# Kernel tuning notes

Hardware: AMD Instinct MI355X
Metric: run time of the kernel (lower is better)

## Reference

```python
import jax, jax.numpy as jnp
import numpy as np

B, L, E, H = 1, 2048, 512, 8
D = E // H


def setup_inputs() -> dict:
    key = jax.random.key(0)
    k0, k1, k2 = jax.random.split(key, 3)
    x = jax.random.normal(k0, (B, L, E), jnp.float32)
    W_qkv = jax.random.normal(k1, (E, 3 * E), jnp.float32) / np.sqrt(E).astype(np.float32)
    b_qkv = jnp.zeros((3 * E,), jnp.float32)
    W_out = jax.random.normal(k2, (E, E), jnp.float32) / np.sqrt(E).astype(np.float32)
    b_out = jnp.zeros((E,), jnp.float32)
    return {"x": x, "W_qkv": W_qkv, "b_qkv": b_qkv, "W_out": W_out, "b_out": b_out}


def reference(x, W_qkv, b_qkv, W_out, b_out):
    num_heads = H
    eps = 1e-6
    b, l, e = x.shape
    d = e // num_heads
    qkv = x @ W_qkv + b_qkv                      # [B, L, 3E]
    q, k, v = jnp.split(qkv, 3, axis=-1)
    q = q.reshape(b, l, num_heads, d).transpose(0, 2, 1, 3)  # [B,H,L,D]
    k = k.reshape(b, l, num_heads, d).transpose(0, 2, 1, 3)
    v = v.reshape(b, l, num_heads, d).transpose(0, 2, 1, 3)
    pos = jnp.arange(l, dtype=jnp.float32).reshape(1, 1, l, 1)
    cos_w = jnp.cos(jnp.pi / 2 * pos / l)
    sin_w = jnp.sin(jnp.pi / 2 * pos / l)
    q_prime = jax.nn.relu(q)
    k_prime = jax.nn.relu(k)

    def branch(w):
        qw = q_prime * w                          # [B,H,L,D]
        kw = k_prime * w
        kv = jnp.einsum('bhld,bhle->bhlde', kw, v)  # causal running KV state
        kv_cum = jnp.cumsum(kv, axis=2)
        ctx = jnp.einsum('bhld,bhlde->bhle', qw, kv_cum)
        nrm = jnp.einsum('bhld,bhld->bhl', qw, jnp.cumsum(kw, axis=2))
        return ctx, nrm

    ctx_cos, nrm_cos = branch(cos_w)
    ctx_sin, nrm_sin = branch(sin_w)
    out = (ctx_cos + ctx_sin) / ((nrm_cos + nrm_sin)[..., None] + eps)
    out = out.transpose(0, 2, 1, 3).reshape(b, l, e)
    return out @ W_out + b_out
```

## Files before the change

### kernel.cpp

```cpp
#include <hip/hip_runtime.h>

constexpr int L_SEQ = 2048;
constexpr int E_DIM = 512;
constexpr int H_NUM = 8;
constexpr int QKV_W = 3 * E_DIM;
constexpr int NC = 32;
constexpr float PI_HALF = 1.5707963267948966f;

typedef __attribute__((ext_vector_type(8))) short bf16x8;
typedef __attribute__((ext_vector_type(4))) float f32x4;
typedef __attribute__((ext_vector_type(4))) short short4v;

__device__ __forceinline__ short f2bf(float f) {
  union { float f; unsigned int u; } v; v.f = f;
  unsigned int r = v.u + 0x7fffu + ((v.u >> 16) & 1u);
  return (short)(r >> 16);
}
__device__ __forceinline__ float bf2f(short s) {
  union { unsigned int u; float f; } v;
  v.u = ((unsigned int)(unsigned short)s) << 16;
  return v.f;
}

__device__ __forceinline__ void glds16(const void* g, void* l) {
  __builtin_amdgcn_global_load_lds(
      (const __attribute__((address_space(1))) unsigned int*)g,
      (__attribute__((address_space(3))) unsigned int*)l, 16, 0, 0);
}

template <int WTM, int WTN, bool OB>
__global__ __launch_bounds__(256) void gemm_mfma_bf16(
    const short* __restrict__ A, const short* __restrict__ Bt,
    const float* __restrict__ bias, void* __restrict__ Cout,
    int M, int N, int K) {
  constexpr int BM = WTM * 32;
  constexpr int BN = WTN * 32;
  __shared__ short As[BM * 32];
  __shared__ short Bs[BN * 32];

  const int t = threadIdx.x;
  const int wave = t >> 6;
  const int lane = t & 63;
  const int quad = lane >> 4;
  const int lr = lane & 15;

  const int row0 = blockIdx.y * BM;
  const int col0 = blockIdx.x * BN;
  const int wrow = (wave >> 1) * (BM / 2);
  const int wcol = (wave & 1) * (BN / 2);

  f32x4 acc[WTM][WTN];
#pragma unroll
  for (int m = 0; m < WTM; ++m)
#pragma unroll
    for (int n = 0; n < WTN; ++n) acc[m][n] = (f32x4){0.f, 0.f, 0.f, 0.f};

  for (int k0 = 0; k0 < K; k0 += 32) {
#pragma unroll
    for (int p = wave; p < BM / 16; p += 4) {
      const int idx = p * 64 + lane;
      glds16(A + (size_t)(row0 + (idx >> 2)) * K + k0 + (idx & 3) * 8, As + p * 512);
    }
#pragma unroll
    for (int p = wave; p < BN / 16; p += 4) {
      const int idx = p * 64 + lane;
      glds16(Bt + (size_t)(col0 + (idx >> 2)) * K + k0 + (idx & 3) * 8, Bs + p * 512);
    }
    __syncthreads();

    bf16x8 af[WTM], bf_[WTN];
#pragma unroll
    for (int m = 0; m < WTM; ++m)
      af[m] = *(const bf16x8*)(As + (wrow + m * 16 + lr) * 32 + quad * 8);
#pragma unroll
    for (int n = 0; n < WTN; ++n)
      bf_[n] = *(const bf16x8*)(Bs + (wcol + n * 16 + lr) * 32 + quad * 8);
#pragma unroll
    for (int m = 0; m < WTM; ++m)
#pragma unroll
      for (int n = 0; n < WTN; ++n)
        acc[m][n] = __builtin_amdgcn_mfma_f32_16x16x32_bf16(af[m], bf_[n], acc[m][n], 0, 0, 0);
    __syncthreads();
  }

#pragma unroll
  for (int m = 0; m < WTM; ++m) {
#pragma unroll
    for (int n = 0; n < WTN; ++n) {
      const int col = col0 + wcol + n * 16 + lr;
      const int rowb = row0 + wrow + m * 16 + quad * 4;
      const float bb = bias[col];
#pragma unroll
      for (int r = 0; r < 4; ++r) {
        const float val = acc[m][n][r] + bb;
        if (OB)
          ((short*)Cout)[(size_t)(rowb + r) * N + col] = f2bf(val);
        else
          ((float*)Cout)[(size_t)(rowb + r) * N + col] = val;
      }
    }
  }
}

__global__ __launch_bounds__(256) void prep_kernel(
    const float* __restrict__ x, const float* __restrict__ W_qkv,
    const float* __restrict__ W_out, short* __restrict__ xb,
    short* __restrict__ Wqkv_t, short* __restrict__ Wout_t) {
  const int b = blockIdx.x;
  if (b < 1024) {
    const int i = b * 256 + threadIdx.x;
    const float4 v = ((const float4*)x)[i];
    short4v o;
    o.x = f2bf(v.x); o.y = f2bf(v.y); o.z = f2bf(v.z); o.w = f2bf(v.w);
    ((short4v*)xb)[i] = o;
    return;
  }
  __shared__ float tile[32][33];
  const float* W; short* Wt; int R, Cc, c0, r0;
  if (b < 1792) {
    const int bb = b - 1024;
    W = W_qkv; Wt = Wqkv_t; R = E_DIM; Cc = QKV_W;
    c0 = (bb % 48) * 32; r0 = (bb / 48) * 32;
  } else {
    const int bb = b - 1792;
    W = W_out; Wt = Wout_t; R = E_DIM; Cc = E_DIM;
    c0 = (bb % 16) * 32; r0 = (bb / 16) * 32;
  }
  const int tx = threadIdx.x & 31, ty = threadIdx.x >> 5;
  for (int i = ty; i < 32; i += 8) tile[i][tx] = W[(size_t)(r0 + i) * Cc + c0 + tx];
  __syncthreads();
  for (int i = ty; i < 32; i += 8)
    Wt[(size_t)(c0 + i) * R + r0 + tx] = f2bf(tile[tx][i]);
}

__global__ __launch_bounds__(256) void chunk_kv_mfma(
    const short* __restrict__ qkvb, short* __restrict__ Sb, float* __restrict__ ksum) {
  const int c = blockIdx.x, h = blockIdx.y;
  __shared__ short kT[128][72];
  __shared__ short vT[64][72];
  const int t = threadIdx.x;
  const int w = t >> 6, lane = t & 63, lr = lane & 15, quad = lane >> 4;

#pragma unroll
  for (int r = 0; r < 16; ++r) {
    const int i = w + 4 * r, d = lane;
    const short* row = qkvb + (size_t)(c * 64 + i) * QKV_W;
    const float kv_ = fmaxf(bf2f(row[E_DIM + h * 64 + d]), 0.f);
    const float v_ = bf2f(row[2 * E_DIM + h * 64 + d]);
    const float th = PI_HALF * (float)(c * 64 + i) / (float)L_SEQ;
    kT[d][i] = f2bf(kv_ * __cosf(th));
    kT[64 + d][i] = f2bf(kv_ * __sinf(th));
    vT[d][i] = f2bf(v_);
  }
  __syncthreads();

  f32x4 acc[8];
#pragma unroll
  for (int n = 0; n < 8; ++n) acc[n] = (f32x4){0.f, 0.f, 0.f, 0.f};
#pragma unroll
  for (int kk = 0; kk < 2; ++kk) {
    const bf16x8 av = *(const bf16x8*)&vT[16 * w + lr][kk * 32 + quad * 8];
#pragma unroll
    for (int n = 0; n < 8; ++n) {
      const bf16x8 bv = *(const bf16x8*)&kT[16 * n + lr][kk * 32 + quad * 8];
      acc[n] = __builtin_amdgcn_mfma_f32_16x16x32_bf16(av, bv, acc[n], 0, 0, 0);
    }
  }

  short* Sc = Sb + ((size_t)(h * NC + c)) * 8192;
#pragma unroll
  for (int n = 0; n < 8; ++n) {
    const int dd = 16 * n + lr;
#pragma unroll
    for (int r = 0; r < 4; ++r) {
      const int e = 16 * w + quad * 4 + r;
      Sc[(size_t)e * 128 + dd] = f2bf(acc[n][r]);
    }
  }

  if (t < 128) {
    float s = 0.f;
#pragma unroll
    for (int j = 0; j < 8; ++j) {
      const bf16x8 kv8 = *(const bf16x8*)&kT[t][j * 8];
#pragma unroll
      for (int q = 0; q < 8; ++q) s += bf2f(kv8[q]);
    }
    ksum[(size_t)(h * NC + c) * 128 + t] = s;
  }
}

__global__ __launch_bounds__(256) void scan_kernel(
    const short* __restrict__ Sb, short* __restrict__ Spb,
    const float* __restrict__ ksum, float* __restrict__ ksumP) {
  const int h = blockIdx.y;
  const int g = (blockIdx.x * 256 + threadIdx.x) * 8;
  float run[8];
#pragma unroll
  for (int q = 0; q < 8; ++q) run[q] = 0.f;
#pragma unroll
  for (int c = 0; c < NC; ++c) {
    const size_t off = ((size_t)(h * NC + c)) * 8192 + g;
    const bf16x8 v8 = *(const bf16x8*)(Sb + off);
    bf16x8 o;
#pragma unroll
    for (int q = 0; q < 8; ++q) o[q] = f2bf(run[q]);
    *(bf16x8*)(Spb + off) = o;
#pragma unroll
    for (int q = 0; q < 8; ++q) run[q] += bf2f(v8[q]);
  }
  if (blockIdx.x == 0 && threadIdx.x < 128) {
    const int d = threadIdx.x;
    float r2 = 0.f;
#pragma unroll
    for (int c = 0; c < NC; ++c) {
      const size_t off = (size_t)(h * NC + c) * 128 + d;
      ksumP[off] = r2;
      r2 += ksum[off];
    }
  }
}

__global__ __launch_bounds__(256) void chunk_out_mfma(
    const short* __restrict__ qkvb, const short* __restrict__ Spb,
    const float* __restrict__ ksumP, short* __restrict__ attn) {
  const int c = blockIdx.x, h = blockIdx.y;
  __shared__ short Qc[64][136];
  __shared__ short Kc[64][136];
  __shared__ short Am[64][72];
  __shared__ short vT[64][72];
  __shared__ float nrmP[64][4];
  __shared__ float nrmA[64];
  const int t = threadIdx.x;
  const int w = t >> 6, lane = t & 63, lr = lane & 15, quad = lane >> 4;

#pragma unroll
  for (int r = 0; r < 16; ++r) {
    const int i = w + 4 * r, d = lane;
    const short* row = qkvb + (size_t)(c * 64 + i) * QKV_W;
    const float q_ = fmaxf(bf2f(row[h * 64 + d]), 0.f);
    const float k_ = fmaxf(bf2f(row[E_DIM + h * 64 + d]), 0.f);
    const float v_ = bf2f(row[2 * E_DIM + h * 64 + d]);
    const float th = PI_HALF * (float)(c * 64 + i) / (float)L_SEQ;
    const float cw = __cosf(th), sw = __sinf(th);
    Qc[i][d] = f2bf(q_ * cw);
    Qc[i][64 + d] = f2bf(q_ * sw);
    Kc[i][d] = f2bf(k_ * cw);
    Kc[i][64 + d] = f2bf(k_ * sw);
    vT[d][i] = f2bf(v_);
  }
  __syncthreads();

  bf16x8 av[4];
#pragma unroll
  for (int kk = 0; kk < 4; ++kk)
    av[kk] = *(const bf16x8*)&Qc[16 * w + lr][kk * 32 + quad * 8];

  const short* Spc = Spb + ((size_t)(h * NC + c)) * 8192;
  f32x4 acc_c[4];
#pragma unroll
  for (int n = 0; n < 4; ++n) acc_c[n] = (f32x4){0.f, 0.f, 0.f, 0.f};
#pragma unroll
  for (int kk = 0; kk < 4; ++kk) {
#pragma unroll
    for (int n = 0; n < 4; ++n) {
      const bf16x8 bv = *(const bf16x8*)(Spc + (size_t)(16 * n + lr) * 128 + kk * 32 + quad * 8);
      acc_c[n] = __builtin_amdgcn_mfma_f32_16x16x32_bf16(av[kk], bv, acc_c[n], 0, 0, 0);
    }
  }

  f32x4 acc_a[4];
#pragma unroll
  for (int n = 0; n < 4; ++n) acc_a[n] = (f32x4){0.f, 0.f, 0.f, 0.f};
#pragma unroll
  for (int kk = 0; kk < 4; ++kk) {
#pragma unroll
    for (int n = 0; n < 4; ++n) {
      const bf16x8 bv = *(const bf16x8*)&Kc[16 * n + lr][kk * 32 + quad * 8];
      acc_a[n] = __builtin_amdgcn_mfma_f32_16x16x32_bf16(av[kk], bv, acc_a[n], 0, 0, 0);
    }
  }
#pragma unroll
  for (int n = 0; n < 4; ++n) {
#pragma unroll
    for (int r = 0; r < 4; ++r) {
      const int gi = 16 * w + quad * 4 + r;
      const int gj = 16 * n + lr;
      float val = (gj <= gi) ? acc_a[n][r] : 0.f;
      Am[gi][gj] = f2bf(val);
      float s = val;
      s += __shfl_xor(s, 1, 64);
      s += __shfl_xor(s, 2, 64);
      s += __shfl_xor(s, 4, 64);
      s += __shfl_xor(s, 8, 64);
      if (lr == 0) nrmP[gi][n] = s;
    }
  }
  __syncthreads();

#pragma unroll
  for (int kk = 0; kk < 2; ++kk) {
    const bf16x8 am = *(const bf16x8*)&Am[16 * w + lr][kk * 32 + quad * 8];
#pragma unroll
    for (int n = 0; n < 4; ++n) {
      const bf16x8 bv = *(const bf16x8*)&vT[16 * n + lr][kk * 32 + quad * 8];
      acc_c[n] = __builtin_amdgcn_mfma_f32_16x16x32_bf16(am, bv, acc_c[n], 0, 0, 0);
    }
  }

  {
    const int i = t >> 2, p = t & 3;
    const float* Kp = ksumP + (size_t)(h * NC + c) * 128;
    float dot = 0.f;
#pragma unroll
    for (int jj = 0; jj < 32; ++jj) {
      const int dd = p * 32 + jj;
      dot += bf2f(Qc[i][dd]) * Kp[dd];
    }
    nrmP[i][p] += dot;
  }
  __syncthreads();
  if (t < 64) nrmA[t] = nrmP[t][0] + nrmP[t][1] + nrmP[t][2] + nrmP[t][3];
  __syncthreads();

#pragma unroll
  for (int n = 0; n < 4; ++n) {
#pragma unroll
    for (int r = 0; r < 4; ++r) {
      const int gi = 16 * w + quad * 4 + r;
      const int e = 16 * n + lr;
      const float val = acc_c[n][r] / (nrmA[gi] + 1e-6f);
      attn[(size_t)(c * 64 + gi) * E_DIM + h * 64 + e] = f2bf(val);
    }
  }
}

extern "C" void kernel_launch(void* const* d_in, const int* in_sizes, int n_in,
                              void* d_out, int out_size, void* d_ws, size_t ws_size,
                              hipStream_t stream) {
  (void)in_sizes; (void)n_in; (void)out_size; (void)ws_size;
  const float* x     = (const float*)d_in[0];
  const float* W_qkv = (const float*)d_in[1];
  const float* b_qkv = (const float*)d_in[2];
  const float* W_out = (const float*)d_in[3];
  const float* b_out = (const float*)d_in[4];
  float* out = (float*)d_out;

  short* sws = (short*)d_ws;
  short* qkvb   = sws;
  short* Sb     = qkvb + 3145728;
  short* Spb    = Sb + 2097152;
  short* attn_b = Spb + 2097152;
  short* xb     = attn_b + 1048576;
  short* Wqkv_t = xb + 1048576;
  short* Wout_t = Wqkv_t + 786432;
  float* ksum   = (float*)(Wout_t + 262144);
  float* ksumP  = ksum + 32768;

  prep_kernel<<<2048, 256, 0, stream>>>(x, W_qkv, W_out, xb, Wqkv_t, Wout_t);

  gemm_mfma_bf16<2, 2, true><<<dim3(QKV_W / 64, L_SEQ / 64), 256, 0, stream>>>(
      xb, Wqkv_t, b_qkv, qkvb, L_SEQ, QKV_W, E_DIM);

  chunk_kv_mfma<<<dim3(NC, H_NUM), 256, 0, stream>>>(qkvb, Sb, ksum);

  scan_kernel<<<dim3(4, H_NUM), 256, 0, stream>>>(Sb, Spb, ksum, ksumP);

  chunk_out_mfma<<<dim3(NC, H_NUM), 256, 0, stream>>>(qkvb, Spb, ksumP, attn_b);

  gemm_mfma_bf16<1, 2, false><<<dim3(E_DIM / 64, L_SEQ / 32), 256, 0, stream>>>(
      attn_b, Wout_t, b_out, out, L_SEQ, E_DIM, E_DIM);
}
```

Baseline: 109.7 us.

## Fuse all stages into one persistent kernel with software grid barriers

After: 432.0 us. 294% more time.

```diff
diff --git a/kernel.cpp b/kernel.cpp
--- a/kernel.cpp
+++ b/kernel.cpp
@@ -5,11 +5,11 @@
 constexpr int H_NUM = 8;
 constexpr int QKV_W = 3 * E_DIM;
 constexpr int NC = 32;
+constexpr int NBLK = 512;
 constexpr float PI_HALF = 1.5707963267948966f;
 
 typedef __attribute__((ext_vector_type(8))) short bf16x8;
 typedef __attribute__((ext_vector_type(4))) float f32x4;
-typedef __attribute__((ext_vector_type(4))) short short4v;
 
 __device__ __forceinline__ short f2bf(float f) {
   union { float f; unsigned int u; } v; v.f = f;
@@ -28,24 +28,31 @@
       (__attribute__((address_space(3))) unsigned int*)l, 16, 0, 0);
 }
 
+__device__ __forceinline__ void grid_sync(unsigned* bar) {
+  __syncthreads();
+  if (threadIdx.x == 0) {
+    unsigned gen = __hip_atomic_load(&bar[1], __ATOMIC_ACQUIRE, __HIP_MEMORY_SCOPE_AGENT);
+    unsigned prev = __hip_atomic_fetch_add(&bar[0], 1u, __ATOMIC_ACQ_REL, __HIP_MEMORY_SCOPE_AGENT);
+    if (prev == (unsigned)NBLK - 1u) {
+      __hip_atomic_store(&bar[0], 0u, __ATOMIC_RELAXED, __HIP_MEMORY_SCOPE_AGENT);
+      __hip_atomic_fetch_add(&bar[1], 1u, __ATOMIC_ACQ_REL, __HIP_MEMORY_SCOPE_AGENT);
+    } else {
+      while (__hip_atomic_load(&bar[1], __ATOMIC_ACQUIRE, __HIP_MEMORY_SCOPE_AGENT) == gen)
+        __builtin_amdgcn_s_sleep(2);
+    }
+  }
+  __syncthreads();
+}
+
 template <int WTM, int WTN, bool OB>
-__global__ __launch_bounds__(256) void gemm_mfma_bf16(
+__device__ __forceinline__ void gemm_tile(
     const short* __restrict__ A, const short* __restrict__ Bt,
     const float* __restrict__ bias, void* __restrict__ Cout,
-    int M, int N, int K) {
+    int N, int K, int row0, int col0, short* As, short* Bs) {
   constexpr int BM = WTM * 32;
   constexpr int BN = WTN * 32;
-  __shared__ short As[BM * 32];
-  __shared__ short Bs[BN * 32];
-
   const int t = threadIdx.x;
-  const int wave = t >> 6;
-  const int lane = t & 63;
-  const int quad = lane >> 4;
-  const int lr = lane & 15;
-
-  const int row0 = blockIdx.y * BM;
-  const int col0 = blockIdx.x * BN;
+  const int wave = t >> 6, lane = t & 63, quad = lane >> 4, lr = lane & 15;
   const int wrow = (wave >> 1) * (BM / 2);
   const int wcol = (wave & 1) * (BN / 2);
 
@@ -102,236 +109,261 @@
   }
 }
 
-__global__ __launch_bounds__(256) void prep_kernel(
+__global__ __launch_bounds__(256, 2) void mega_kernel(
     const float* __restrict__ x, const float* __restrict__ W_qkv,
-    const float* __restrict__ W_out, short* __restrict__ xb,
-    short* __restrict__ Wqkv_t, short* __restrict__ Wout_t) {
-  const int b = blockIdx.x;
-  if (b < 1024) {
-    const int i = b * 256 + threadIdx.x;
-    const float4 v = ((const float4*)x)[i];
-    short4v o;
-    o.x = f2bf(v.x); o.y = f2bf(v.y); o.z = f2bf(v.z); o.w = f2bf(v.w);
-    ((short4v*)xb)[i] = o;
-    return;
-  }
-  __shared__ float tile[32][33];
-  const float* W; short* Wt; int R, Cc, c0, r0;
-  if (b < 1792) {
-    const int bb = b - 1024;
-    W = W_qkv; Wt = Wqkv_t; R = E_DIM; Cc = QKV_W;
-    c0 = (bb % 48) * 32; r0 = (bb / 48) * 32;
-  } else {
-    const int bb = b - 1792;
-    W = W_out; Wt = Wout_t; R = E_DIM; Cc = E_DIM;
-    c0 = (bb % 16) * 32; r0 = (bb / 16) * 32;
-  }
-  const int tx = threadIdx.x & 31, ty = threadIdx.x >> 5;
-  for (int i = ty; i < 32; i += 8) tile[i][tx] = W[(size_t)(r0 + i) * Cc + c0 + tx];
-  __syncthreads();
-  for (int i = ty; i < 32; i += 8)
-    Wt[(size_t)(c0 + i) * R + r0 + tx] = f2bf(tile[tx][i]);
-}
-
-__global__ __launch_bounds__(256) void chunk_kv_mfma(
-    const short* __restrict__ qkvb, short* __restrict__ Sb, float* __restrict__ ksum) {
-  const int c = blockIdx.x, h = blockIdx.y;
-  __shared__ short kT[128][72];
-  __shared__ short vT[64][72];
+    const float* __restrict__ b_qkv, const float* __restrict__ W_out,
+    const float* __restrict__ b_out, float* __restrict__ out,
+    short* __restrict__ xb, short* __restrict__ Wqkv_t, short* __restrict__ Wout_t,
+    short* __restrict__ qkvb, short* __restrict__ Sb, short* __restrict__ Spb,
+    short* __restrict__ attn_b, float* __restrict__ ksum, float* __restrict__ ksumP,
+    unsigned* bar) {
+  __shared__ __align__(16) char smem[49920];
+  const int bid = blockIdx.x;
   const int t = threadIdx.x;
   const int w = t >> 6, lane = t & 63, lr = lane & 15, quad = lane >> 4;
 
-#pragma unroll
-  for (int r = 0; r < 16; ++r) {
-    const int i = w + 4 * r, d = lane;
-    const short* row = qkvb + (size_t)(c * 64 + i) * QKV_W;
-    const float kv_ = fmaxf(bf2f(row[E_DIM + h * 64 + d]), 0.f);
-    const float v_ = bf2f(row[2 * E_DIM + h * 64 + d]);
-    const float th = PI_HALF * (float)(c * 64 + i) / (float)L_SEQ;
-    kT[d][i] = f2bf(kv_ * __cosf(th));
-    kT[64 + d][i] = f2bf(kv_ * __sinf(th));
-    vT[d][i] = f2bf(v_);
-  }
-  __syncthreads();
-
-  f32x4 acc[8];
-#pragma unroll
-  for (int n = 0; n < 8; ++n) acc[n] = (f32x4){0.f, 0.f, 0.f, 0.f};
-#pragma unroll
-  for (int kk = 0; kk < 2; ++kk) {
-    const bf16x8 av = *(const bf16x8*)&vT[16 * w + lr][kk * 32 + quad * 8];
-#pragma unroll
-    for (int n = 0; n < 8; ++n) {
-      const bf16x8 bv = *(const bf16x8*)&kT[16 * n + lr][kk * 32 + quad * 8];
-      acc[n] = __builtin_amdgcn_mfma_f32_16x16x32_bf16(av, bv, acc[n], 0, 0, 0);
-    }
-  }
-
-  short* Sc = Sb + ((size_t)(h * NC + c)) * 8192;
-#pragma unroll
-  for (int n = 0; n < 8; ++n) {
-    const int dd = 16 * n + lr;
-#pragma unroll
-    for (int r = 0; r < 4; ++r) {
-      const int e = 16 * w + quad * 4 + r;
-      Sc[(size_t)e * 128 + dd] = f2bf(acc[n][r]);
-    }
-  }
-
-  if (t < 128) {
-    float s = 0.f;
-#pragma unroll
-    for (int j = 0; j < 8; ++j) {
-      const bf16x8 kv8 = *(const bf16x8*)&kT[t][j * 8];
-#pragma unroll
-      for (int q = 0; q < 8; ++q) s += bf2f(kv8[q]);
-    }
-    ksum[(size_t)(h * NC + c) * 128 + t] = s;
-  }
-}
-
-__global__ __launch_bounds__(256) void scan_kernel(
-    const short* __restrict__ Sb, short* __restrict__ Spb,
-    const float* __restrict__ ksum, float* __restrict__ ksumP) {
-  const int h = blockIdx.y;
-  const int g = (blockIdx.x * 256 + threadIdx.x) * 8;
-  float run[8];
-#pragma unroll
-  for (int q = 0; q < 8; ++q) run[q] = 0.f;
-#pragma unroll
-  for (int c = 0; c < NC; ++c) {
-    const size_t off = ((size_t)(h * NC + c)) * 8192 + g;
-    const bf16x8 v8 = *(const bf16x8*)(Sb + off);
+  {
+    const int g = bid * 256 + t;
+    const float4 v0 = ((const float4*)x)[g * 2];
+    const float4 v1 = ((const float4*)x)[g * 2 + 1];
     bf16x8 o;
-#pragma unroll
-    for (int q = 0; q < 8; ++q) o[q] = f2bf(run[q]);
-    *(bf16x8*)(Spb + off) = o;
-#pragma unroll
-    for (int q = 0; q < 8; ++q) run[q] += bf2f(v8[q]);
-  }
-  if (blockIdx.x == 0 && threadIdx.x < 128) {
-    const int d = threadIdx.x;
-    float r2 = 0.f;
-#pragma unroll
-    for (int c = 0; c < NC; ++c) {
-      const size_t off = (size_t)(h * NC + c) * 128 + d;
-      ksumP[off] = r2;
-      r2 += ksum[off];
-    }
-  }
-}
-
-__global__ __launch_bounds__(256) void chunk_out_mfma(
-    const short* __restrict__ qkvb, const short* __restrict__ Spb,
-    const float* __restrict__ ksumP, short* __restrict__ attn) {
-  const int c = blockIdx.x, h = blockIdx.y;
-  __shared__ short Qc[64][136];
-  __shared__ short Kc[64][136];
-  __shared__ short Am[64][72];
-  __shared__ short vT[64][72];
-  __shared__ float nrmP[64][4];
-  __shared__ float nrmA[64];
-  const int t = threadIdx.x;
-  const int w = t >> 6, lane = t & 63, lr = lane & 15, quad = lane >> 4;
-
-#pragma unroll
-  for (int r = 0; r < 16; ++r) {
-    const int i = w + 4 * r, d = lane;
-    const short* row = qkvb + (size_t)(c * 64 + i) * QKV_W;
-    const float q_ = fmaxf(bf2f(row[h * 64 + d]), 0.f);
-    const float k_ = fmaxf(bf2f(row[E_DIM + h * 64 + d]), 0.f);
-    const float v_ = bf2f(row[2 * E_DIM + h * 64 + d]);
-    const float th = PI_HALF * (float)(c * 64 + i) / (float)L_SEQ;
-    const float cw = __cosf(th), sw = __sinf(th);
-    Qc[i][d] = f2bf(q_ * cw);
-    Qc[i][64 + d] = f2bf(q_ * sw);
-    Kc[i][d] = f2bf(k_ * cw);
-    Kc[i][64 + d] = f2bf(k_ * sw);
-    vT[d][i] = f2bf(v_);
-  }
-  __syncthreads();
-
-  bf16x8 av[4];
-#pragma unroll
-  for (int kk = 0; kk < 4; ++kk)
-    av[kk] = *(const bf16x8*)&Qc[16 * w + lr][kk * 32 + quad * 8];
-
-  const short* Spc = Spb + ((size_t)(h * NC + c)) * 8192;
-  f32x4 acc_c[4];
-#pragma unroll
-  for (int n = 0; n < 4; ++n) acc_c[n] = (f32x4){0.f, 0.f, 0.f, 0.f};
-#pragma unroll
-  for (int kk = 0; kk < 4; ++kk) {
+    o[0] = f2bf(v0.x); o[1] = f2bf(v0.y); o[2] = f2bf(v0.z); o[3] = f2bf(v0.w);
+    o[4] = f2bf(v1.x); o[5] = f2bf(v1.y); o[6] = f2bf(v1.z); o[7] = f2bf(v1.w);
+    *(bf16x8*)(xb + (size_t)g * 8) = o;
+
+    float (*tile)[33] = (float(*)[33])smem;
+    const int tx = t & 31, ty = t >> 5;
+#pragma unroll
+    for (int rep = 0; rep < 2; ++rep) {
+      const int j = bid * 2 + rep;
+      const float* W; short* Wt; int Cc, c0, r0;
+      if (j < 768) {
+        W = W_qkv; Wt = Wqkv_t; Cc = QKV_W;
+        c0 = (j % 48) * 32; r0 = (j / 48) * 32;
+      } else {
+        const int jj = j - 768;
+        W = W_out; Wt = Wout_t; Cc = E_DIM;
+        c0 = (jj % 16) * 32; r0 = (jj / 16) * 32;
+      }
+      __syncthreads();
+      for (int i = ty; i < 32; i += 8) tile[i][tx] = W[(size_t)(r0 + i) * Cc + c0 + tx];
+      __syncthreads();
+      for (int i = ty; i < 32; i += 8)
+        Wt[(size_t)(c0 + i) * E_DIM + r0 + tx] = f2bf(tile[tx][i]);
+    }
+  }
+  grid_sync(bar);
+
+  {
+    short* As = (short*)smem;
+    short* Bs = (short*)(smem + 4096);
+    const int col0 = (bid & 15) * 96;
+    const int row0 = (bid >> 4) * 64;
+    gemm_tile<2, 3, true>(xb, Wqkv_t, b_qkv, qkvb, QKV_W, E_DIM, row0, col0, As, Bs);
+  }
+  grid_sync(bar);
+
+  {
+    const int half = bid >> 8, rem = bid & 255, h = rem >> 5, c = rem & 31;
+    short (*kT)[72] = (short(*)[72])smem;
+    short (*vT)[72] = (short(*)[72])(smem + 9216);
+#pragma unroll
+    for (int r = 0; r < 16; ++r) {
+      const int i = w + 4 * r, d = lane;
+      const short* row = qkvb + (size_t)(c * 64 + i) * QKV_W;
+      const float kv_ = fmaxf(bf2f(row[E_DIM + h * 64 + d]), 0.f);
+      const float v_ = bf2f(row[2 * E_DIM + h * 64 + d]);
+      const float th = PI_HALF * (float)(c * 64 + i) / (float)L_SEQ;
+      const float wgt = half ? __sinf(th) : __cosf(th);
+      kT[d][i] = f2bf(kv_ * wgt);
+      vT[d][i] = f2bf(v_);
+    }
+    __syncthreads();
+
+    f32x4 acc[4];
+#pragma unroll
+    for (int n = 0; n < 4; ++n) acc[n] = (f32x4){0.f, 0.f, 0.f, 0.f};
+#pragma unroll
+    for (int kk = 0; kk < 2; ++kk) {
+      const bf16x8 av = *(const bf16x8*)&vT[16 * w + lr][kk * 32 + quad * 8];
+#pragma unroll
+      for (int n = 0; n < 4; ++n) {
+        const bf16x8 bv = *(const bf16x8*)&kT[16 * n + lr][kk * 32 + quad * 8];
+        acc[n] = __builtin_amdgcn_mfma_f32_16x16x32_bf16(av, bv, acc[n], 0, 0, 0);
+      }
+    }
+    short* Sc = Sb + ((size_t)(h * NC + c)) * 8192;
 #pragma unroll
     for (int n = 0; n < 4; ++n) {
-      const bf16x8 bv = *(const bf16x8*)(Spc + (size_t)(16 * n + lr) * 128 + kk * 32 + quad * 8);
-      acc_c[n] = __builtin_amdgcn_mfma_f32_16x16x32_bf16(av[kk], bv, acc_c[n], 0, 0, 0);
-    }
-  }
-
-  f32x4 acc_a[4];
-#pragma unroll
-  for (int n = 0; n < 4; ++n) acc_a[n] = (f32x4){0.f, 0.f, 0.f, 0.f};
-#pragma unroll
-  for (int kk = 0; kk < 4; ++kk) {
+      const int dd = 64 * half + 16 * n + lr;
+#pragma unroll
+      for (int r = 0; r < 4; ++r) {
+        const int e = 16 * w + quad * 4 + r;
+        Sc[(size_t)e * 128 + dd] = f2bf(acc[n][r]);
+      }
+    }
+    if (t < 64) {
+      float s = 0.f;
+#pragma unroll
+      for (int j = 0; j < 8; ++j) {
+        const bf16x8 kv8 = *(const bf16x8*)&kT[t][j * 8];
+#pragma unroll
+        for (int q = 0; q < 8; ++q) s += bf2f(kv8[q]);
+      }
+      ksum[(size_t)(h * NC + c) * 128 + 64 * half + t] = s;
+    }
+  }
+  grid_sync(bar);
+
+  {
+    const int gid = bid * 256 + t;
+    if (gid < 8192) {
+      const int hh = gid >> 10, grp = gid & 1023;
+      float run[8];
+#pragma unroll
+      for (int q = 0; q < 8; ++q) run[q] = 0.f;
+#pragma unroll
+      for (int c = 0; c < NC; ++c) {
+        const size_t off = ((size_t)(hh * NC + c)) * 8192 + grp * 8;
+        const bf16x8 v8 = *(const bf16x8*)(Sb + off);
+        bf16x8 o;
+#pragma unroll
+        for (int q = 0; q < 8; ++q) o[q] = f2bf(run[q]);
+        *(bf16x8*)(Spb + off) = o;
+#pragma unroll
+        for (int q = 0; q < 8; ++q) run[q] += bf2f(v8[q]);
+      }
+    } else if (gid < 9216) {
+      const int j = gid - 8192, hh = j >> 7, d = j & 127;
+      float r2 = 0.f;
+#pragma unroll
+      for (int c = 0; c < NC; ++c) {
+        const size_t off = (size_t)(hh * NC + c) * 128 + d;
+        ksumP[off] = r2;
+        r2 += ksum[off];
+      }
+    }
+  }
+  grid_sync(bar);
+
+  {
+    const int half = bid >> 8, rem = bid & 255, h = rem >> 5, c = rem & 31;
+    short (*Qc)[136] = (short(*)[136])smem;
+    short (*Kc)[136] = (short(*)[136])(smem + 17408);
+    short (*Am)[72]  = (short(*)[72])(smem + 34816);
+    short (*vTl)[72] = (short(*)[72])(smem + 44032);
+    float (*nrmP)[4] = (float(*)[4])(smem + 48640);
+    float* nrmA      = (float*)(smem + 49664);
+
+#pragma unroll
+    for (int r = 0; r < 16; ++r) {
+      const int i = w + 4 * r, d = lane;
+      const short* row = qkvb + (size_t)(c * 64 + i) * QKV_W;
+      const float q_ = fmaxf(bf2f(row[h * 64 + d]), 0.f);
+      const float k_ = fmaxf(bf2f(row[E_DIM + h * 64 + d]), 0.f);
+      const float v_ = bf2f(row[2 * E_DIM + h * 64 + d]);
+      const float th = PI_HALF * (float)(c * 64 + i) / (float)L_SEQ;
+      const float cw = __cosf(th), sw = __sinf(th);
+      Qc[i][d] = f2bf(q_ * cw);
+      Qc[i][64 + d] = f2bf(q_ * sw);
+      Kc[i][d] = f2bf(k_ * cw);
+      Kc[i][64 + d] = f2bf(k_ * sw);
+      if ((d >> 5) == half) vTl[d & 31][i] = f2bf(v_);
+    }
+    __syncthreads();
+
+    bf16x8 av[4];
+#pragma unroll
+    for (int kk = 0; kk < 4; ++kk)
+      av[kk] = *(const bf16x8*)&Qc[16 * w + lr][kk * 32 + quad * 8];
+
+    f32x4 acc_a[4];
+#pragma unroll
+    for (int n = 0; n < 4; ++n) acc_a[n] = (f32x4){0.f, 0.f, 0.f, 0.f};
+#pragma unroll
+    for (int kk = 0; kk < 4; ++kk) {
+#pragma unroll
+      for (int n = 0; n < 4; ++n) {
+        const bf16x8 bv = *(const bf16x8*)&Kc[16 * n + lr][kk * 32 + quad * 8];
+        acc_a[n] = __builtin_amdgcn_mfma_f32_16x16x32_bf16(av[kk], bv, acc_a[n], 0, 0, 0);
+      }
+    }
 #pragma unroll
     for (int n = 0; n < 4; ++n) {
-      const bf16x8 bv = *(const bf16x8*)&Kc[16 * n + lr][kk * 32 + quad * 8];
-      acc_a[n] = __builtin_amdgcn_mfma_f32_16x16x32_bf16(av[kk], bv, acc_a[n], 0, 0, 0);
-    }
-  }
-#pragma unroll
-  for (int n = 0; n < 4; ++n) {
-#pragma unroll
-    for (int r = 0; r < 4; ++r) {
-      const int gi = 16 * w + quad * 4 + r;
-      const int gj = 16 * n + lr;
-      float val = (gj <= gi) ? acc_a[n][r] : 0.f;
-      Am[gi][gj] = f2bf(val);
-      float s = val;
-      s += __shfl_xor(s, 1, 64);
-      s += __shfl_xor(s, 2, 64);
-      s += __shfl_xor(s, 4, 64);
-      s += __shfl_xor(s, 8, 64);
-      if (lr == 0) nrmP[gi][n] = s;
-    }
-  }
-  __syncthreads();
-
-#pragma unroll
-  for (int kk = 0; kk < 2; ++kk) {
-    const bf16x8 am = *(const bf16x8*)&Am[16 * w + lr][kk * 32 + quad * 8];
-#pragma unroll
-    for (int n = 0; n < 4; ++n) {
-      const bf16x8 bv = *(const bf16x8*)&vT[16 * n + lr][kk * 32 + quad * 8];
-      acc_c[n] = __builtin_amdgcn_mfma_f32_16x16x32_bf16(am, bv, acc_c[n], 0, 0, 0);
-    }
-  }
-
-  {
-    const int i = t >> 2, p = t & 3;
-    const float* Kp = ksumP + (size_t)(h * NC + c) * 128;
-    float dot = 0.f;
-#pragma unroll
-    for (int jj = 0; jj < 32; ++jj) {
-      const int dd = p * 32 + jj;
-      dot += bf2f(Qc[i][dd]) * Kp[dd];
-    }
-    nrmP[i][p] += dot;
-  }
-  __syncthreads();
-  if (t < 64) nrmA[t] = nrmP[t][0] + nrmP[t][1] + nrmP[t][2] + nrmP[t][3];
-  __syncthreads();
-
-#pragma unroll
-  for (int n = 0; n < 4; ++n) {
-#pragma unroll
-    for (int r = 0; r < 4; ++r) {
-      const int gi = 16 * w + quad * 4 + r;
-      const int e = 16 * n + lr;
-      const float val = acc_c[n][r] / (nrmA[gi] + 1e-6f);
-      attn[(size_t)(c * 64 + gi) * E_DIM + h * 64 + e] = f2bf(val);
-    }
+#pragma unroll
+      for (int r = 0; r < 4; ++r) {
+        const int gi = 16 * w + quad * 4 + r;
+        const int gj = 16 * n + lr;
+        float val = (gj <= gi) ? acc_a[n][r] : 0.f;
+        Am[gi][gj] = f2bf(val);
+        float s = val;
+        s += __shfl_xor(s, 1, 64);
+        s += __shfl_xor(s, 2, 64);
+        s += __shfl_xor(s, 4, 64);
+        s += __shfl_xor(s, 8, 64);
+        if (lr == 0) nrmP[gi][n] = s;
+      }
+    }
+
+    const short* Spc = Spb + ((size_t)(h * NC + c)) * 8192;
+    f32x4 acc_c[2];
+#pragma unroll
+    for (int n = 0; n < 2; ++n) acc_c[n] = (f32x4){0.f, 0.f, 0.f, 0.f};
+#pragma unroll
+    for (int kk = 0; kk < 4; ++kk) {
+#pragma unroll
+      for (int n2 = 0; n2 < 2; ++n2) {
+        const int e = 32 * half + 16 * n2 + lr;
+        const bf16x8 bv = *(const bf16x8*)(Spc + (size_t)e * 128 + kk * 32 + quad * 8);
+        acc_c[n2] = __builtin_amdgcn_mfma_f32_16x16x32_bf16(av[kk], bv, acc_c[n2], 0, 0, 0);
+      }
+    }
+    __syncthreads();
+
+#pragma unroll
+    for (int kk = 0; kk < 2; ++kk) {
+      const bf16x8 am = *(const bf16x8*)&Am[16 * w + lr][kk * 32 + quad * 8];
+#pragma unroll
+      for (int n2 = 0; n2 < 2; ++n2) {
+        const bf16x8 bv = *(const bf16x8*)&vTl[16 * n2 + lr][kk * 32 + quad * 8];
+        acc_c[n2] = __builtin_amdgcn_mfma_f32_16x16x32_bf16(am, bv, acc_c[n2], 0, 0, 0);
+      }
+    }
+
+    {
+      const int i = t >> 2, p = t & 3;
+      const float* Kp = ksumP + (size_t)(h * NC + c) * 128;
+      float dot = 0.f;
+#pragma unroll
+      for (int jj = 0; jj < 32; ++jj) {
+        const int dd = p * 32 + jj;
+        dot += bf2f(Qc[i][dd]) * Kp[dd];
+      }
+      nrmP[i][p] += dot;
+    }
+    __syncthreads();
+    if (t < 64) nrmA[t] = nrmP[t][0] + nrmP[t][1] + nrmP[t][2] + nrmP[t][3];
+    __syncthreads();
+
+#pragma unroll
+    for (int n2 = 0; n2 < 2; ++n2) {
+#pragma unroll
+      for (int r = 0; r < 4; ++r) {
+        const int gi = 16 * w + quad * 4 + r;
+        const int e = 32 * half + 16 * n2 + lr;
+        const float val = acc_c[n2][r] / (nrmA[gi] + 1e-6f);
+        attn_b[(size_t)(c * 64 + gi) * E_DIM + h * 64 + e] = f2bf(val);
+      }
+    }
+  }
+  grid_sync(bar);
+
+  {
+    short* As = (short*)smem;
+    short* Bs = (short*)(smem + 4096);
+    const int col0 = (bid & 15) * 32;
+    const int row0 = (bid >> 4) * 64;
+    gemm_tile<2, 1, false>(attn_b, Wout_t, b_out, out, E_DIM, E_DIM, row0, col0, As, Bs);
   }
 }
 
@@ -346,7 +378,8 @@
   const float* b_out = (const float*)d_in[4];
   float* out = (float*)d_out;
 
-  short* sws = (short*)d_ws;
+  unsigned* bar = (unsigned*)d_ws;
+  short* sws    = (short*)((char*)d_ws + 128);
   short* qkvb   = sws;
   short* Sb     = qkvb + 3145728;
   short* Spb    = Sb + 2097152;
@@ -357,17 +390,9 @@
   float* ksum   = (float*)(Wout_t + 262144);
   float* ksumP  = ksum + 32768;
 
-  prep_kernel<<<2048, 256, 0, stream>>>(x, W_qkv, W_out, xb, Wqkv_t, Wout_t);
-
-  gemm_mfma_bf16<2, 2, true><<<dim3(QKV_W / 64, L_SEQ / 64), 256, 0, stream>>>(
-      xb, Wqkv_t, b_qkv, qkvb, L_SEQ, QKV_W, E_DIM);
-
-  chunk_kv_mfma<<<dim3(NC, H_NUM), 256, 0, stream>>>(qkvb, Sb, ksum);
-
-  scan_kernel<<<dim3(4, H_NUM), 256, 0, stream>>>(Sb, Spb, ksum, ksumP);
-
-  chunk_out_mfma<<<dim3(NC, H_NUM), 256, 0, stream>>>(qkvb, Spb, ksumP, attn_b);
-
-  gemm_mfma_bf16<1, 2, false><<<dim3(E_DIM / 64, L_SEQ / 32), 256, 0, stream>>>(
-      attn_b, Wout_t, b_out, out, L_SEQ, E_DIM, E_DIM);
-}
+  hipMemsetAsync(bar, 0, 8, stream);
+
+  mega_kernel<<<NBLK, 256, 0, stream>>>(
+      x, W_qkv, b_qkv, W_out, b_out, out,
+      xb, Wqkv_t, Wout_t, qkvb, Sb, Spb, attn_b, ksum, ksumP, bar);
+}
```

## Fuse QKV projection GEMM into chunk_kv and chunk_out kernels

Applied to the files above, without the earlier changes.

Result: slower. 117.7 us (+7.2%).

```diff
diff --git a/kernel.cpp b/kernel.cpp
--- a/kernel.cpp
+++ b/kernel.cpp
@@ -39,11 +39,7 @@
   __shared__ short Bs[BN * 32];
 
   const int t = threadIdx.x;
-  const int wave = t >> 6;
-  const int lane = t & 63;
-  const int quad = lane >> 4;
-  const int lr = lane & 15;
-
+  const int wave = t >> 6, lane = t & 63, quad = lane >> 4, lr = lane & 15;
   const int row0 = blockIdx.y * BM;
   const int col0 = blockIdx.x * BN;
   const int wrow = (wave >> 1) * (BM / 2);
@@ -116,68 +112,126 @@
     return;
   }
   __shared__ float tile[32][33];
-  const float* W; short* Wt; int R, Cc, c0, r0;
+  const float* W; short* Wt; int Cc, c0, r0;
   if (b < 1792) {
     const int bb = b - 1024;
-    W = W_qkv; Wt = Wqkv_t; R = E_DIM; Cc = QKV_W;
+    W = W_qkv; Wt = Wqkv_t; Cc = QKV_W;
     c0 = (bb % 48) * 32; r0 = (bb / 48) * 32;
   } else {
     const int bb = b - 1792;
-    W = W_out; Wt = Wout_t; R = E_DIM; Cc = E_DIM;
+    W = W_out; Wt = Wout_t; Cc = E_DIM;
     c0 = (bb % 16) * 32; r0 = (bb / 16) * 32;
   }
   const int tx = threadIdx.x & 31, ty = threadIdx.x >> 5;
   for (int i = ty; i < 32; i += 8) tile[i][tx] = W[(size_t)(r0 + i) * Cc + c0 + tx];
   __syncthreads();
   for (int i = ty; i < 32; i += 8)
-    Wt[(size_t)(c0 + i) * R + r0 + tx] = f2bf(tile[tx][i]);
-}
-
-__global__ __launch_bounds__(256) void chunk_kv_mfma(
-    const short* __restrict__ qkvb, short* __restrict__ Sb, float* __restrict__ ksum) {
+    Wt[(size_t)(c0 + i) * E_DIM + r0 + tx] = f2bf(tile[tx][i]);
+}
+
+__global__ __launch_bounds__(256) void chunk_kv_fused(
+    const short* __restrict__ xb, const short* __restrict__ Wqkv_t,
+    const float* __restrict__ b_qkv, short* __restrict__ Sb,
+    float* __restrict__ ksum) {
   const int c = blockIdx.x, h = blockIdx.y;
-  __shared__ short kT[128][72];
-  __shared__ short vT[64][72];
+  __shared__ __align__(16) char smem[39936];
+  short* As = (short*)smem;
+  short* Bs = (short*)(smem + 4096);
+  short (*kT)[72] = (short(*)[72])(smem + 12288);
+  short (*vT)[72] = (short(*)[72])(smem + 30720);
+
   const int t = threadIdx.x;
-  const int w = t >> 6, lane = t & 63, lr = lane & 15, quad = lane >> 4;
-
-#pragma unroll
-  for (int r = 0; r < 16; ++r) {
-    const int i = w + 4 * r, d = lane;
-    const short* row = qkvb + (size_t)(c * 64 + i) * QKV_W;
-    const float kv_ = fmaxf(bf2f(row[E_DIM + h * 64 + d]), 0.f);
-    const float v_ = bf2f(row[2 * E_DIM + h * 64 + d]);
-    const float th = PI_HALF * (float)(c * 64 + i) / (float)L_SEQ;
-    kT[d][i] = f2bf(kv_ * __cosf(th));
-    kT[64 + d][i] = f2bf(kv_ * __sinf(th));
-    vT[d][i] = f2bf(v_);
-  }
-  __syncthreads();
-
-  f32x4 acc[8];
-#pragma unroll
-  for (int n = 0; n < 8; ++n) acc[n] = (f32x4){0.f, 0.f, 0.f, 0.f};
+  const int wave = t >> 6, lane = t & 63, quad = lane >> 4, lr = lane & 15;
+  const int wrow = (wave >> 1) * 32;
+  const int wcol = (wave & 1) * 64;
+
+  f32x4 acc[2][4];
+#pragma unroll
+  for (int m = 0; m < 2; ++m)
+#pragma unroll
+    for (int n = 0; n < 4; ++n) acc[m][n] = (f32x4){0.f, 0.f, 0.f, 0.f};
+
+  for (int k0 = 0; k0 < E_DIM; k0 += 32) {
+    {
+      const int idx = wave * 64 + lane;
+      glds16(xb + (size_t)(c * 64 + (idx >> 2)) * E_DIM + k0 + (idx & 3) * 8, As + wave * 512);
+    }
+#pragma unroll
+    for (int p = wave; p < 8; p += 4) {
+      const int idx = p * 64 + lane;
+      const int rr = idx >> 2;
+      const int g = h * 64 + rr + ((rr < 64) ? E_DIM : 2 * E_DIM - 64);
+      glds16(Wqkv_t + (size_t)g * E_DIM + k0 + (idx & 3) * 8, Bs + p * 512);
+    }
+    __syncthreads();
+    bf16x8 af[2], bf_[4];
+#pragma unroll
+    for (int m = 0; m < 2; ++m)
+      af[m] = *(const bf16x8*)(As + (wrow + m * 16 + lr) * 32 + quad * 8);
+#pragma unroll
+    for (int n = 0; n < 4; ++n)
+      bf_[n] = *(const bf16x8*)(Bs + (wcol + n * 16 + lr) * 32 + quad * 8);
+#pragma unroll
+    for (int m = 0; m < 2; ++m)
+#pragma unroll
+      for (int n = 0; n < 4; ++n)
+        acc[m][n] = __builtin_amdgcn_mfma_f32_16x16x32_bf16(af[m], bf_[n], acc[m][n], 0, 0, 0);
+    __syncthreads();
+  }
+
+  float cwv[2][4], swv[2][4];
+#pragma unroll
+  for (int m = 0; m < 2; ++m)
+#pragma unroll
+    for (int r = 0; r < 4; ++r) {
+      const int i = wrow + m * 16 + quad * 4 + r;
+      const float th = PI_HALF * (float)(c * 64 + i) / (float)L_SEQ;
+      __sincosf(th, &swv[m][r], &cwv[m][r]);
+    }
+#pragma unroll
+  for (int n = 0; n < 4; ++n) {
+    const int j = wcol + n * 16 + lr;
+    const float bb = b_qkv[h * 64 + j + ((j < 64) ? E_DIM : 2 * E_DIM - 64)];
+#pragma unroll
+    for (int m = 0; m < 2; ++m) {
+#pragma unroll
+      for (int r = 0; r < 4; ++r) {
+        const int i = wrow + m * 16 + quad * 4 + r;
+        const float val = acc[m][n][r] + bb;
+        if (j < 64) {
+          const float kv = fmaxf(val, 0.f);
+          kT[j][i] = f2bf(kv * cwv[m][r]);
+          kT[64 + j][i] = f2bf(kv * swv[m][r]);
+        } else {
+          vT[j - 64][i] = f2bf(val);
+        }
+      }
+    }
+  }
+  __syncthreads();
+
+  f32x4 sacc[8];
+#pragma unroll
+  for (int n = 0; n < 8; ++n) sacc[n] = (f32x4){0.f, 0.f, 0.f, 0.f};
 #pragma unroll
   for (int kk = 0; kk < 2; ++kk) {
-    const bf16x8 av = *(const bf16x8*)&vT[16 * w + lr][kk * 32 + quad * 8];
+    const bf16x8 av = *(const bf16x8*)&vT[16 * wave + lr][kk * 32 + quad * 8];
 #pragma unroll
     for (int n = 0; n < 8; ++n) {
       const bf16x8 bv = *(const bf16x8*)&kT[16 * n + lr][kk * 32 + quad * 8];
-      acc[n] = __builtin_amdgcn_mfma_f32_16x16x32_bf16(av, bv, acc[n], 0, 0, 0);
-    }
-  }
-
+      sacc[n] = __builtin_amdgcn_mfma_f32_16x16x32_bf16(av, bv, sacc[n], 0, 0, 0);
+    }
+  }
   short* Sc = Sb + ((size_t)(h * NC + c)) * 8192;
 #pragma unroll
   for (int n = 0; n < 8; ++n) {
     const int dd = 16 * n + lr;
 #pragma unroll
     for (int r = 0; r < 4; ++r) {
-      const int e = 16 * w + quad * 4 + r;
-      Sc[(size_t)e * 128 + dd] = f2bf(acc[n][r]);
-    }
-  }
-
+      const int e = 16 * wave + quad * 4 + r;
+      Sc[(size_t)e * 128 + dd] = f2bf(sacc[n][r]);
+    }
+  }
   if (t < 128) {
     float s = 0.f;
 #pragma unroll
@@ -221,53 +275,99 @@
   }
 }
 
-__global__ __launch_bounds__(256) void chunk_out_mfma(
-    const short* __restrict__ qkvb, const short* __restrict__ Spb,
+__global__ __launch_bounds__(256) void chunk_out_fused(
+    const short* __restrict__ xb, const short* __restrict__ Wqkv_t,
+    const float* __restrict__ b_qkv, const short* __restrict__ Spb,
     const float* __restrict__ ksumP, short* __restrict__ attn) {
   const int c = blockIdx.x, h = blockIdx.y;
-  __shared__ short Qc[64][136];
-  __shared__ short Kc[64][136];
-  __shared__ short Am[64][72];
-  __shared__ short vT[64][72];
-  __shared__ float nrmP[64][4];
-  __shared__ float nrmA[64];
+  __shared__ __align__(16) char smem[60416];
+  short* As = (short*)smem;
+  short* Bs = (short*)(smem + 4096);
+  short (*Am)[72]  = (short(*)[72])smem;
+  float (*nrmP)[4] = (float(*)[4])(smem + 9216);
+  float* nrmA      = (float*)(smem + 10240);
+  short (*Qc)[136] = (short(*)[136])(smem + 16384);
+  short (*Kc)[136] = (short(*)[136])(smem + 33792);
+  short (*vT)[72]  = (short(*)[72])(smem + 51200);
+
   const int t = threadIdx.x;
-  const int w = t >> 6, lane = t & 63, lr = lane & 15, quad = lane >> 4;
-
-#pragma unroll
-  for (int r = 0; r < 16; ++r) {
-    const int i = w + 4 * r, d = lane;
-    const short* row = qkvb + (size_t)(c * 64 + i) * QKV_W;
-    const float q_ = fmaxf(bf2f(row[h * 64 + d]), 0.f);
-    const float k_ = fmaxf(bf2f(row[E_DIM + h * 64 + d]), 0.f);
-    const float v_ = bf2f(row[2 * E_DIM + h * 64 + d]);
-    const float th = PI_HALF * (float)(c * 64 + i) / (float)L_SEQ;
-    const float cw = __cosf(th), sw = __sinf(th);
-    Qc[i][d] = f2bf(q_ * cw);
-    Qc[i][64 + d] = f2bf(q_ * sw);
-    Kc[i][d] = f2bf(k_ * cw);
-    Kc[i][64 + d] = f2bf(k_ * sw);
-    vT[d][i] = f2bf(v_);
+  const int wave = t >> 6, lane = t & 63, quad = lane >> 4, lr = lane & 15;
+  const int wrow = (wave >> 1) * 32;
+  const int wcol = (wave & 1) * 96;
+
+  f32x4 acc[2][6];
+#pragma unroll
+  for (int m = 0; m < 2; ++m)
+#pragma unroll
+    for (int n = 0; n < 6; ++n) acc[m][n] = (f32x4){0.f, 0.f, 0.f, 0.f};
+
+  for (int k0 = 0; k0 < E_DIM; k0 += 32) {
+    {
+      const int idx = wave * 64 + lane;
+      glds16(xb + (size_t)(c * 64 + (idx >> 2)) * E_DIM + k0 + (idx & 3) * 8, As + wave * 512);
+    }
+#pragma unroll
+    for (int p = wave; p < 12; p += 4) {
+      const int idx = p * 64 + lane;
+      const int rr = idx >> 2;
+      const int g = h * 64 + rr + ((rr < 64) ? 0 : (rr < 128) ? E_DIM - 64 : 2 * E_DIM - 128);
+      glds16(Wqkv_t + (size_t)g * E_DIM + k0 + (idx & 3) * 8, Bs + p * 512);
+    }
+    __syncthreads();
+    bf16x8 af[2], bf_[6];
+#pragma unroll
+    for (int m = 0; m < 2; ++m)
+      af[m] = *(const bf16x8*)(As + (wrow + m * 16 + lr) * 32 + quad * 8);
+#pragma unroll
+    for (int n = 0; n < 6; ++n)
+      bf_[n] = *(const bf16x8*)(Bs + (wcol + n * 16 + lr) * 32 + quad * 8);
+#pragma unroll
+    for (int m = 0; m < 2; ++m)
+#pragma unroll
+      for (int n = 0; n < 6; ++n)
+        acc[m][n] = __builtin_amdgcn_mfma_f32_16x16x32_bf16(af[m], bf_[n], acc[m][n], 0, 0, 0);
+    __syncthreads();
+  }
+
+  float cwv[2][4], swv[2][4];
+#pragma unroll
+  for (int m = 0; m < 2; ++m)
+#pragma unroll
+    for (int r = 0; r < 4; ++r) {
+      const int i = wrow + m * 16 + quad * 4 + r;
+      const float th = PI_HALF * (float)(c * 64 + i) / (float)L_SEQ;
+      __sincosf(th, &swv[m][r], &cwv[m][r]);
+    }
+#pragma unroll
+  for (int n = 0; n < 6; ++n) {
+    const int j = wcol + n * 16 + lr;
+    const float bb = b_qkv[h * 64 + j + ((j < 64) ? 0 : (j < 128) ? E_DIM - 64 : 2 * E_DIM - 128)];
+#pragma unroll
+    for (int m = 0; m < 2; ++m) {
+#pragma unroll
+      for (int r = 0; r < 4; ++r) {
+        const int i = wrow + m * 16 + quad * 4 + r;
+        const float val = acc[m][n][r] + bb;
+        if (j < 64) {
+          const float qv = fmaxf(val, 0.f);
+          Qc[i][j] = f2bf(qv * cwv[m][r]);
+          Qc[i][64 + j] = f2bf(qv * swv[m][r]);
+        } else if (j < 128) {
+          const float kv = fmaxf(val, 0.f);
+          Kc[i][j - 64] = f2bf(kv * cwv[m][r]);
+          Kc[i][64 + (j - 64)] = f2bf(kv * swv[m][r]);
+        } else {
+          vT[j - 128][i] = f2bf(val);
+        }
+      }
+    }
   }
   __syncthreads();
 
   bf16x8 av[4];
 #pragma unroll
   for (int kk = 0; kk < 4; ++kk)
-    av[kk] = *(const bf16x8*)&Qc[16 * w + lr][kk * 32 + quad * 8];
-
-  const short* Spc = Spb + ((size_t)(h * NC + c)) * 8192;
-  f32x4 acc_c[4];
-#pragma unroll
-  for (int n = 0; n < 4; ++n) acc_c[n] = (f32x4){0.f, 0.f, 0.f, 0.f};
-#pragma unroll
-  for (int kk = 0; kk < 4; ++kk) {
-#pragma unroll
-    for (int n = 0; n < 4; ++n) {
-      const bf16x8 bv = *(const bf16x8*)(Spc + (size_t)(16 * n + lr) * 128 + kk * 32 + quad * 8);
-      acc_c[n] = __builtin_amdgcn_mfma_f32_16x16x32_bf16(av[kk], bv, acc_c[n], 0, 0, 0);
-    }
-  }
+    av[kk] = *(const bf16x8*)&Qc[16 * wave + lr][kk * 32 + quad * 8];
 
   f32x4 acc_a[4];
 #pragma unroll
@@ -284,7 +384,7 @@
   for (int n = 0; n < 4; ++n) {
 #pragma unroll
     for (int r = 0; r < 4; ++r) {
-      const int gi = 16 * w + quad * 4 + r;
+      const int gi = 16 * wave + quad * 4 + r;
       const int gj = 16 * n + lr;
       float val = (gj <= gi) ? acc_a[n][r] : 0.f;
       Am[gi][gj] = f2bf(val);
@@ -296,11 +396,24 @@
       if (lr == 0) nrmP[gi][n] = s;
     }
   }
+
+  const short* Spc = Spb + ((size_t)(h * NC + c)) * 8192;
+  f32x4 acc_c[4];
+#pragma unroll
+  for (int n = 0; n < 4; ++n) acc_c[n] = (f32x4){0.f, 0.f, 0.f, 0.f};
+#pragma unroll
+  for (int kk = 0; kk < 4; ++kk) {
+#pragma unroll
+    for (int n = 0; n < 4; ++n) {
+      const bf16x8 bv = *(const bf16x8*)(Spc + (size_t)(16 * n + lr) * 128 + kk * 32 + quad * 8);
+      acc_c[n] = __builtin_amdgcn_mfma_f32_16x16x32_bf16(av[kk], bv, acc_c[n], 0, 0, 0);
+    }
+  }
   __syncthreads();
 
 #pragma unroll
   for (int kk = 0; kk < 2; ++kk) {
-    const bf16x8 am = *(const bf16x8*)&Am[16 * w + lr][kk * 32 + quad * 8];
+    const bf16x8 am = *(const bf16x8*)&Am[16 * wave + lr][kk * 32 + quad * 8];
 #pragma unroll
     for (int n = 0; n < 4; ++n) {
       const bf16x8 bv = *(const bf16x8*)&vT[16 * n + lr][kk * 32 + quad * 8];
@@ -327,7 +440,7 @@
   for (int n = 0; n < 4; ++n) {
 #pragma unroll
     for (int r = 0; r < 4; ++r) {
-      const int gi = 16 * w + quad * 4 + r;
+      const int gi = 16 * wave + quad * 4 + r;
       const int e = 16 * n + lr;
       const float val = acc_c[n][r] / (nrmA[gi] + 1e-6f);
       attn[(size_t)(c * 64 + gi) * E_DIM + h * 64 + e] = f2bf(val);
@@ -347,8 +460,7 @@
   float* out = (float*)d_out;
 
   short* sws = (short*)d_ws;
-  short* qkvb   = sws;
-  short* Sb     = qkvb + 3145728;
+  short* Sb     = sws;
   short* Spb    = Sb + 2097152;
   short* attn_b = Spb + 2097152;
   short* xb     = attn_b + 1048576;
@@ -359,14 +471,12 @@
 
   prep_kernel<<<2048, 256, 0, stream>>>(x, W_qkv, W_out, xb, Wqkv_t, Wout_t);
 
-  gemm_mfma_bf16<2, 2, true><<<dim3(QKV_W / 64, L_SEQ / 64), 256, 0, stream>>>(
-      xb, Wqkv_t, b_qkv, qkvb, L_SEQ, QKV_W, E_DIM);
-
-  chunk_kv_mfma<<<dim3(NC, H_NUM), 256, 0, stream>>>(qkvb, Sb, ksum);
+  chunk_kv_fused<<<dim3(NC, H_NUM), 256, 0, stream>>>(xb, Wqkv_t, b_qkv, Sb, ksum);
 
   scan_kernel<<<dim3(4, H_NUM), 256, 0, stream>>>(Sb, Spb, ksum, ksumP);
 
-  chunk_out_mfma<<<dim3(NC, H_NUM), 256, 0, stream>>>(qkvb, Spb, ksumP, attn_b);
+  chunk_out_fused<<<dim3(NC, H_NUM), 256, 0, stream>>>(
+      xb, Wqkv_t, b_qkv, Spb, ksumP, attn_b);
 
   gemm_mfma_bf16<1, 2, false><<<dim3(E_DIM / 64, L_SEQ / 32), 256, 0, stream>>>(
       attn_b, Wout_t, b_out, out, L_SEQ, E_DIM, E_DIM);
```
